# Kernel tuning notes

Measured on AMD Instinct MI355X. Metric: run time of the kernel, lower is better.

The kernel has to match this reference:

```python
import jax, jax.numpy as jnp
import numpy as np

B, F, N = 128, 256, 2000

def setup_inputs() -> dict:
    key = jax.random.key(0)
    ks = jax.random.split(key, 10)
    s = 0.05
    return {
        'nfeature': jax.random.normal(ks[0], (B, F, N, 1), jnp.float32),
        'last_current': jax.random.randint(ks[1], (B, 2), 0, N, jnp.int32),
        'Wg': jax.random.normal(ks[2], (F, F), jnp.float32) * s,
        'bg': jax.random.normal(ks[3], (F,), jnp.float32) * s,
        'Wnode': jax.random.normal(ks[4], (3 * F, F), jnp.float32) * s,
        'bnode': jax.random.normal(ks[5], (3 * F,), jnp.float32) * s,
        'Wlc': jax.random.normal(ks[6], (F, 2 * F), jnp.float32) * s,
        'blc': jax.random.normal(ks[7], (F,), jnp.float32) * s,
        'Wproj': jax.random.normal(ks[8], (F, F), jnp.float32) * s,
        'bproj': jax.random.normal(ks[9], (F,), jnp.float32) * s,
    }

def reference(nfeature, last_current, Wg, bg, Wnode, bnode, Wlc, blc, Wproj, bproj):
    # nfeature: [B, F, N, 1]
    x = nfeature[..., 0]                                  # [B, F, N]
    f = x.shape[1]
    scale = 1.0 / jnp.sqrt(jnp.asarray(f, x.dtype))
    # global fixed query: max over nodes then Linear
    glb = jnp.max(x, axis=2)                              # [B, F]
    Q = glb @ Wg.T + bg                                   # [B, F]
    # node embeddings via 1x1 conv == channel GEMM, split into K, V, logit_K
    kvl = jnp.einsum('bfn,gf->bgn', x, Wnode) + bnode[None, :, None]  # [B, 3F, N]
    K, V, Klog = jnp.split(kvl, 3, axis=1)                # each [B, F, N]
    # gather last/current city features
    lc = jnp.take_along_axis(x, last_current[:, None, :], axis=2)     # [B, F, 2]
    context = jnp.concatenate([lc[:, :, 0], lc[:, :, 1]], axis=1)     # [B, 2F]
    cQ = context @ Wlc.T + blc + Q                        # [B, F]
    # attention: single query over N keys
    ucj = jnp.einsum('bf,bfn->bn', cQ, K) * scale         # [B, N]
    attn = jax.nn.softmax(ucj, axis=1)
    nc = jnp.einsum('bn,bfn->bf', attn, V)                # [B, F]
    nc = nc @ Wproj.T + bproj                             # [B, F]
    logits = jnp.einsum('bf,bfn->bn', nc, Klog) * scale   # [B, N]
    return jnp.tanh(logits) * 10.0
```

## Files before the change

kernel.cpp:

```cpp
#include <hip/hip_runtime.h>
#include <hip/hip_fp16.h>
#include <math.h>

#define BB 128
#define FF 256
#define NN 2000

typedef float f32x4 __attribute__((ext_vector_type(4)));
union H8 { f32x4 v; __half2 h[4]; };

__global__ __launch_bounds__(256) void k_convmax(const float* __restrict__ x,
                                                 __half* __restrict__ xh,
                                                 float* __restrict__ glb) {
    int row  = (blockIdx.x << 2) | (threadIdx.x >> 6);
    int lane = threadIdx.x & 63;
    const f32x4* src = (const f32x4*)(x + (size_t)row * NN);
    f32x4*       dst = (f32x4*)(xh + (size_t)row * NN);
    float m = -INFINITY;
    for (int i = lane; i < 250; i += 64) {
        f32x4 a = __builtin_nontemporal_load(src + 2 * i);
        f32x4 b = __builtin_nontemporal_load(src + 2 * i + 1);
        m = fmaxf(m, fmaxf(fmaxf(a.x, a.y), fmaxf(a.z, a.w)));
        m = fmaxf(m, fmaxf(fmaxf(b.x, b.y), fmaxf(b.z, b.w)));
        H8 o;
        o.h[0] = __floats2half2_rn(a.x, a.y);
        o.h[1] = __floats2half2_rn(a.z, a.w);
        o.h[2] = __floats2half2_rn(b.x, b.y);
        o.h[3] = __floats2half2_rn(b.z, b.w);
        dst[i] = o.v;
    }
#pragma unroll
    for (int off = 32; off; off >>= 1) m = fmaxf(m, __shfl_xor(m, off));
    if (!lane) glb[row] = m;
}

__global__ __launch_bounds__(256) void k_prep(
    const float* __restrict__ x, const int* __restrict__ lc,
    const float* __restrict__ glb,
    const float* __restrict__ Wg, const float* __restrict__ bg,
    const float* __restrict__ Wnode, const float* __restrict__ bnode,
    const float* __restrict__ Wlc, const float* __restrict__ blc,
    float* __restrict__ cK, float* __restrict__ cK0)
{
    int b = blockIdx.x;
    int f = threadIdx.x;
    __shared__ float s_glb[FF], s_ctx[2 * FF], s_cQ[FF], s_red[FF];
    const float* xb = x + (size_t)b * FF * NN;
    s_glb[f] = glb[b * FF + f];
    int l0 = lc[2 * b], l1 = lc[2 * b + 1];
    s_ctx[f]      = xb[(size_t)f * NN + l0];
    s_ctx[FF + f] = xb[(size_t)f * NN + l1];
    __syncthreads();
    float q = bg[f];
    const float* wg = Wg + (size_t)f * FF;
    for (int j = 0; j < FF; ++j) q = fmaf(wg[j], s_glb[j], q);
    float cq = blc[f] + q;
    const float* wl = Wlc + (size_t)f * 2 * FF;
    for (int j = 0; j < 2 * FF; ++j) cq = fmaf(wl[j], s_ctx[j], cq);
    s_cQ[f]  = cq;
    s_red[f] = cq * bnode[f];
    __syncthreads();
    float ck = 0.f;
    for (int g = 0; g < FF; ++g) ck = fmaf(s_cQ[g], Wnode[(size_t)g * FF + f], ck);
    cK[b * FF + f] = ck;
    for (int s = 128; s > 0; s >>= 1) {
        if (f < s) s_red[f] += s_red[f + s];
        __syncthreads();
    }
    if (f == 0) cK0[b] = s_red[0];
}

__global__ __launch_bounds__(256) void k_ucj(const __half* __restrict__ xh,
                                             const float* __restrict__ cK,
                                             float* __restrict__ u)
{
    int b = blockIdx.x >> 2, s = blockIdx.x & 3;
    int tid = threadIdx.x, w = tid >> 6, lane = tid & 63;
    __shared__ float s_cK[FF];
    __shared__ float s_part[4][512];
    s_cK[tid] = cK[b * FF + tid];
    __syncthreads();
    int n0 = s << 9;
    int nbase = n0 + (lane << 3);
    float a0 = 0, a1 = 0, a2 = 0, a3 = 0, a4 = 0, a5 = 0, a6 = 0, a7 = 0;
    if (nbase < NN) {
        const __half* rp = xh + (size_t)(b * FF + (w << 6)) * NN + nbase;
#pragma unroll 4
        for (int fi = 0; fi < 64; ++fi) {
            H8 hv; hv.v = *(const f32x4*)rp;
            rp += NN;
            float c = s_cK[(w << 6) + fi];
            float2 q0 = __half22float2(hv.h[0]);
            float2 q1 = __half22float2(hv.h[1]);
            float2 q2 = __half22float2(hv.h[2]);
            float2 q3 = __half22float2(hv.h[3]);
            a0 = fmaf(c, q0.x, a0); a1 = fmaf(c, q0.y, a1);
            a2 = fmaf(c, q1.x, a2); a3 = fmaf(c, q1.y, a3);
            a4 = fmaf(c, q2.x, a4); a5 = fmaf(c, q2.y, a5);
            a6 = fmaf(c, q3.x, a6); a7 = fmaf(c, q3.y, a7);
        }
    }
    int cb = lane << 3;
    s_part[w][cb + 0] = a0; s_part[w][cb + 1] = a1;
    s_part[w][cb + 2] = a2; s_part[w][cb + 3] = a3;
    s_part[w][cb + 4] = a4; s_part[w][cb + 5] = a5;
    s_part[w][cb + 6] = a6; s_part[w][cb + 7] = a7;
    __syncthreads();
    for (int c = tid; c < 512; c += 256) {
        int n = n0 + c;
        if (n < NN)
            u[(size_t)b * NN + n] =
                s_part[0][c] + s_part[1][c] + s_part[2][c] + s_part[3][c];
    }
}

__global__ __launch_bounds__(256) void k_softmax(const float* __restrict__ u,
                                                 const float* __restrict__ cK0,
                                                 float* __restrict__ p)
{
    int b = blockIdx.x, tid = threadIdx.x, w = tid >> 6, lane = tid & 63;
    __shared__ float s_red[8];
    float k0 = cK0[b];
    const float scale = 0.0625f;
    float v[8];
    float m = -INFINITY;
#pragma unroll
    for (int j = 0; j < 8; ++j) {
        int n = (j << 8) + tid;
        float t = -INFINITY;
        if (n < NN) t = (u[(size_t)b * NN + n] + k0) * scale;
        v[j] = t;
        m = fmaxf(m, t);
    }
#pragma unroll
    for (int off = 32; off; off >>= 1) m = fmaxf(m, __shfl_xor(m, off));
    if (!lane) s_red[w] = m;
    __syncthreads();
    m = fmaxf(fmaxf(s_red[0], s_red[1]), fmaxf(s_red[2], s_red[3]));
    float sum = 0.f;
#pragma unroll
    for (int j = 0; j < 8; ++j) {
        float e = (v[j] > -INFINITY) ? __expf(v[j] - m) : 0.f;
        v[j] = e;
        sum += e;
    }
#pragma unroll
    for (int off = 32; off; off >>= 1) sum += __shfl_xor(sum, off);
    __syncthreads();
    if (!lane) s_red[w] = sum;
    __syncthreads();
    float inv = 1.0f / (s_red[0] + s_red[1] + s_red[2] + s_red[3]);
#pragma unroll
    for (int j = 0; j < 8; ++j) {
        int n = (j << 8) + tid;
        if (n < NN) p[(size_t)b * NN + n] = v[j] * inv;
    }
}

__global__ __launch_bounds__(256) void k_ypool(const __half* __restrict__ xh,
                                               const float* __restrict__ p,
                                               float* __restrict__ y)
{
    int b = blockIdx.x >> 4, fblk = (blockIdx.x & 15) << 4;
    int tid = threadIdx.x, w = tid >> 6, lane = tid & 63;
    const float4* pb = (const float4*)(p + (size_t)b * NN);
#pragma unroll
    for (int r = 0; r < 4; ++r) {
        int f = fblk + (w << 2) + r;
        const f32x4* row = (const f32x4*)(xh + ((size_t)b * FF + f) * NN);
        float acc = 0.f;
        for (int i = lane; i < 250; i += 64) {
            H8 hv; hv.v = row[i];
            float4 pa = pb[2 * i];
            float4 pc = pb[2 * i + 1];
            float2 q0 = __half22float2(hv.h[0]);
            float2 q1 = __half22float2(hv.h[1]);
            float2 q2 = __half22float2(hv.h[2]);
            float2 q3 = __half22float2(hv.h[3]);
            acc = fmaf(q0.x, pa.x, acc); acc = fmaf(q0.y, pa.y, acc);
            acc = fmaf(q1.x, pa.z, acc); acc = fmaf(q1.y, pa.w, acc);
            acc = fmaf(q2.x, pc.x, acc); acc = fmaf(q2.y, pc.y, acc);
            acc = fmaf(q3.x, pc.z, acc); acc = fmaf(q3.y, pc.w, acc);
        }
#pragma unroll
        for (int off = 32; off; off >>= 1) acc += __shfl_xor(acc, off);
        if (!lane) y[b * FF + f] = acc;
    }
}

__global__ __launch_bounds__(256) void k_dense(
    const float* __restrict__ y,
    const float* __restrict__ Wnode, const float* __restrict__ bnode,
    const float* __restrict__ Wproj, const float* __restrict__ bproj,
    float* __restrict__ cL, float* __restrict__ cL0)
{
    int b = blockIdx.x;
    int f = threadIdx.x;
    int wid = f >> 6, lane = f & 63;
    __shared__ float s_y[FF], s_v[FF], s_red[4];
    s_y[f] = y[b * FF + f];
    __syncthreads();
    float a = bnode[FF + f];
    const float* w = Wnode + (size_t)(FF + f) * FF;
    for (int j = 0; j < FF; ++j) a = fmaf(w[j], s_y[j], a);
    s_v[f] = a;
    __syncthreads();
    float nc2 = bproj[f];
    const float* wp = Wproj + (size_t)f * FF;
    for (int j = 0; j < FF; ++j) nc2 = fmaf(wp[j], s_v[j], nc2);
    __syncthreads();
    s_v[f] = nc2;
    __syncthreads();
    float cl = 0.f;
    for (int g = 0; g < FF; ++g) cl = fmaf(s_v[g], Wnode[(size_t)(2 * FF + g) * FF + f], cl);
    cL[b * FF + f] = cl;
    float t = nc2 * bnode[2 * FF + f];
#pragma unroll
    for (int off = 32; off; off >>= 1) t += __shfl_xor(t, off);
    if (!lane) s_red[wid] = t;
    __syncthreads();
    if (!f) cL0[b] = s_red[0] + s_red[1] + s_red[2] + s_red[3];
}

__global__ __launch_bounds__(256) void k_logits(const __half* __restrict__ xh,
                                                const float* __restrict__ cL,
                                                const float* __restrict__ cL0,
                                                float* __restrict__ out)
{
    int b = blockIdx.x >> 2, s = blockIdx.x & 3;
    int tid = threadIdx.x, w = tid >> 6, lane = tid & 63;
    __shared__ float s_cL[FF];
    __shared__ float s_part[4][512];
    s_cL[tid] = cL[b * FF + tid];
    __syncthreads();
    int n0 = s << 9;
    int nbase = n0 + (lane << 3);
    float a0 = 0, a1 = 0, a2 = 0, a3 = 0, a4 = 0, a5 = 0, a6 = 0, a7 = 0;
    if (nbase < NN) {
        const __half* rp = xh + (size_t)(b * FF + (w << 6)) * NN + nbase;
#pragma unroll 4
        for (int fi = 0; fi < 64; ++fi) {
            H8 hv; hv.v = *(const f32x4*)rp;
            rp += NN;
            float c = s_cL[(w << 6) + fi];
            float2 q0 = __half22float2(hv.h[0]);
            float2 q1 = __half22float2(hv.h[1]);
            float2 q2 = __half22float2(hv.h[2]);
            float2 q3 = __half22float2(hv.h[3]);
            a0 = fmaf(c, q0.x, a0); a1 = fmaf(c, q0.y, a1);
            a2 = fmaf(c, q1.x, a2); a3 = fmaf(c, q1.y, a3);
            a4 = fmaf(c, q2.x, a4); a5 = fmaf(c, q2.y, a5);
            a6 = fmaf(c, q3.x, a6); a7 = fmaf(c, q3.y, a7);
        }
    }
    int cb = lane << 3;
    s_part[w][cb + 0] = a0; s_part[w][cb + 1] = a1;
    s_part[w][cb + 2] = a2; s_part[w][cb + 3] = a3;
    s_part[w][cb + 4] = a4; s_part[w][cb + 5] = a5;
    s_part[w][cb + 6] = a6; s_part[w][cb + 7] = a7;
    __syncthreads();
    float cl0 = cL0[b];
    const float scale = 0.0625f;
    for (int c = tid; c < 512; c += 256) {
        int n = n0 + c;
        if (n < NN) {
            float l = (s_part[0][c] + s_part[1][c] + s_part[2][c] + s_part[3][c] + cl0) * scale;
            out[(size_t)b * NN + n] = tanhf(l) * 10.f;
        }
    }
}

extern "C" void kernel_launch(void* const* d_in, const int* in_sizes, int n_in,
                              void* d_out, int out_size, void* d_ws, size_t ws_size,
                              hipStream_t stream) {
    const float* x     = (const float*)d_in[0];
    const int*   lc    = (const int*)d_in[1];
    const float* Wg    = (const float*)d_in[2];
    const float* bg    = (const float*)d_in[3];
    const float* Wnode = (const float*)d_in[4];
    const float* bnode = (const float*)d_in[5];
    const float* Wlc   = (const float*)d_in[6];
    const float* blc   = (const float*)d_in[7];
    const float* Wproj = (const float*)d_in[8];
    const float* bproj = (const float*)d_in[9];
    float* out = (float*)d_out;

    float* ws   = (float*)d_ws;
    float* glb  = ws + 0;
    float* cK   = ws + 40960;
    float* cK0  = ws + 81920;
    float* u    = ws + 90112;
    float* p    = ws + 360448;
    float* y    = ws + 630784;
    float* cL   = ws + 663552;
    float* cL0  = ws + 696320;
    __half* xh  = (__half*)(ws + (1 << 20));

    k_convmax<<<BB * FF / 4, 256, 0, stream>>>(x, xh, glb);
    k_prep   <<<BB, 256, 0, stream>>>(x, lc, glb, Wg, bg, Wnode, bnode, Wlc, blc, cK, cK0);
    k_ucj    <<<BB * 4, 256, 0, stream>>>(xh, cK, u);
    k_softmax<<<BB, 256, 0, stream>>>(u, cK0, p);
    k_ypool  <<<BB * 16, 256, 0, stream>>>(xh, p, y);
    k_dense  <<<BB, 256, 0, stream>>>(y, Wnode, bnode, Wproj, bproj, cL, cL0);
    k_logits <<<BB * 4, 256, 0, stream>>>(xh, cL, cL0, out);
}
```

Measured before the change: 202.4 us.

## Fuse score, split softmax and pooling into one pass; fuse dense into logits

Merges the score, softmax and attention-pooling kernels into one kernel. Each block computes a local max, sum and partial pooled vector for its 512-node chunk, flash-decoding style. The final kernel combines the four partials, recomputes the dense projection chain per block and then computes the logits, which drops two launches and the u and p round trips. It also splits the accumulators in the prep matvecs. In exchange, the dense GEMVs are now recomputed four times per batch row, and the pooling loop does a 64-lane shuffle reduction for every feature row.

Measured after the change: 219.0 us. 8.2% more time.

```diff
diff --git a/kernel.cpp b/kernel.cpp
--- a/kernel.cpp
+++ b/kernel.cpp
@@ -51,18 +51,31 @@
     s_ctx[f]      = xb[(size_t)f * NN + l0];
     s_ctx[FF + f] = xb[(size_t)f * NN + l1];
     __syncthreads();
-    float q = bg[f];
     const float* wg = Wg + (size_t)f * FF;
-    for (int j = 0; j < FF; ++j) q = fmaf(wg[j], s_glb[j], q);
-    float cq = blc[f] + q;
+    float q0 = 0, q1 = 0, q2 = 0, q3 = 0;
+    for (int j = 0; j < FF; j += 4) {
+        q0 = fmaf(wg[j],     s_glb[j],     q0);
+        q1 = fmaf(wg[j + 1], s_glb[j + 1], q1);
+        q2 = fmaf(wg[j + 2], s_glb[j + 2], q2);
+        q3 = fmaf(wg[j + 3], s_glb[j + 3], q3);
+    }
     const float* wl = Wlc + (size_t)f * 2 * FF;
-    for (int j = 0; j < 2 * FF; ++j) cq = fmaf(wl[j], s_ctx[j], cq);
+    for (int j = 0; j < 2 * FF; j += 4) {
+        q0 = fmaf(wl[j],     s_ctx[j],     q0);
+        q1 = fmaf(wl[j + 1], s_ctx[j + 1], q1);
+        q2 = fmaf(wl[j + 2], s_ctx[j + 2], q2);
+        q3 = fmaf(wl[j + 3], s_ctx[j + 3], q3);
+    }
+    float cq = bg[f] + blc[f] + ((q0 + q1) + (q2 + q3));
     s_cQ[f]  = cq;
     s_red[f] = cq * bnode[f];
     __syncthreads();
-    float ck = 0.f;
-    for (int g = 0; g < FF; ++g) ck = fmaf(s_cQ[g], Wnode[(size_t)g * FF + f], ck);
-    cK[b * FF + f] = ck;
+    float c0 = 0, c1 = 0;
+    for (int g = 0; g < FF; g += 2) {
+        c0 = fmaf(s_cQ[g],     Wnode[(size_t)g * FF + f],       c0);
+        c1 = fmaf(s_cQ[g + 1], Wnode[(size_t)(g + 1) * FF + f], c1);
+    }
+    cK[b * FF + f] = c0 + c1;
     for (int s = 128; s > 0; s >>= 1) {
         if (f < s) s_red[f] += s_red[f + s];
         __syncthreads();
@@ -70,20 +83,27 @@
     if (f == 0) cK0[b] = s_red[0];
 }
 
-__global__ __launch_bounds__(256) void k_ucj(const __half* __restrict__ xh,
-                                             const float* __restrict__ cK,
-                                             float* __restrict__ u)
+__global__ __launch_bounds__(256) void k_attn(
+    const __half* __restrict__ xh,
+    const float* __restrict__ cK, const float* __restrict__ cK0,
+    float* __restrict__ y_part, float* __restrict__ m_part,
+    float* __restrict__ s_part)
 {
     int b = blockIdx.x >> 2, s = blockIdx.x & 3;
     int tid = threadIdx.x, w = tid >> 6, lane = tid & 63;
     __shared__ float s_cK[FF];
-    __shared__ float s_part[4][512];
+    __shared__ float s_acc[4][512];
+    __shared__ float s_p[512];
+    __shared__ float s_red[8];
     s_cK[tid] = cK[b * FF + tid];
     __syncthreads();
+
     int n0 = s << 9;
     int nbase = n0 + (lane << 3);
+    bool valid = nbase < NN;
+
     float a0 = 0, a1 = 0, a2 = 0, a3 = 0, a4 = 0, a5 = 0, a6 = 0, a7 = 0;
-    if (nbase < NN) {
+    if (valid) {
         const __half* rp = xh + (size_t)(b * FF + (w << 6)) * NN + nbase;
 #pragma unroll 4
         for (int fi = 0; fi < 64; ++fi) {
@@ -101,142 +121,139 @@
         }
     }
     int cb = lane << 3;
-    s_part[w][cb + 0] = a0; s_part[w][cb + 1] = a1;
-    s_part[w][cb + 2] = a2; s_part[w][cb + 3] = a3;
-    s_part[w][cb + 4] = a4; s_part[w][cb + 5] = a5;
-    s_part[w][cb + 6] = a6; s_part[w][cb + 7] = a7;
-    __syncthreads();
-    for (int c = tid; c < 512; c += 256) {
-        int n = n0 + c;
-        if (n < NN)
-            u[(size_t)b * NN + n] =
-                s_part[0][c] + s_part[1][c] + s_part[2][c] + s_part[3][c];
-    }
-}
-
-__global__ __launch_bounds__(256) void k_softmax(const float* __restrict__ u,
-                                                 const float* __restrict__ cK0,
-                                                 float* __restrict__ p)
-{
-    int b = blockIdx.x, tid = threadIdx.x, w = tid >> 6, lane = tid & 63;
-    __shared__ float s_red[8];
+    s_acc[w][cb + 0] = a0; s_acc[w][cb + 1] = a1;
+    s_acc[w][cb + 2] = a2; s_acc[w][cb + 3] = a3;
+    s_acc[w][cb + 4] = a4; s_acc[w][cb + 5] = a5;
+    s_acc[w][cb + 6] = a6; s_acc[w][cb + 7] = a7;
+    __syncthreads();
+
+    const float scale = 0.0625f;
     float k0 = cK0[b];
-    const float scale = 0.0625f;
-    float v[8];
-    float m = -INFINITY;
-#pragma unroll
-    for (int j = 0; j < 8; ++j) {
-        int n = (j << 8) + tid;
-        float t = -INFINITY;
-        if (n < NN) t = (u[(size_t)b * NN + n] + k0) * scale;
-        v[j] = t;
-        m = fmaxf(m, t);
-    }
+    float uu0, uu1;
+    {
+        int c0 = tid, c1 = tid + 256;
+        float t0 = s_acc[0][c0] + s_acc[1][c0] + s_acc[2][c0] + s_acc[3][c0];
+        float t1 = s_acc[0][c1] + s_acc[1][c1] + s_acc[2][c1] + s_acc[3][c1];
+        uu0 = (n0 + c0 < NN) ? (t0 + k0) * scale : -INFINITY;
+        uu1 = (n0 + c1 < NN) ? (t1 + k0) * scale : -INFINITY;
+    }
+    float m = fmaxf(uu0, uu1);
 #pragma unroll
     for (int off = 32; off; off >>= 1) m = fmaxf(m, __shfl_xor(m, off));
     if (!lane) s_red[w] = m;
     __syncthreads();
-    m = fmaxf(fmaxf(s_red[0], s_red[1]), fmaxf(s_red[2], s_red[3]));
-    float sum = 0.f;
-#pragma unroll
-    for (int j = 0; j < 8; ++j) {
-        float e = (v[j] > -INFINITY) ? __expf(v[j] - m) : 0.f;
-        v[j] = e;
-        sum += e;
-    }
-#pragma unroll
-    for (int off = 32; off; off >>= 1) sum += __shfl_xor(sum, off);
-    __syncthreads();
-    if (!lane) s_red[w] = sum;
-    __syncthreads();
-    float inv = 1.0f / (s_red[0] + s_red[1] + s_red[2] + s_red[3]);
-#pragma unroll
-    for (int j = 0; j < 8; ++j) {
-        int n = (j << 8) + tid;
-        if (n < NN) p[(size_t)b * NN + n] = v[j] * inv;
-    }
-}
-
-__global__ __launch_bounds__(256) void k_ypool(const __half* __restrict__ xh,
-                                               const float* __restrict__ p,
-                                               float* __restrict__ y)
-{
-    int b = blockIdx.x >> 4, fblk = (blockIdx.x & 15) << 4;
-    int tid = threadIdx.x, w = tid >> 6, lane = tid & 63;
-    const float4* pb = (const float4*)(p + (size_t)b * NN);
-#pragma unroll
-    for (int r = 0; r < 4; ++r) {
-        int f = fblk + (w << 2) + r;
-        const f32x4* row = (const f32x4*)(xh + ((size_t)b * FF + f) * NN);
+    float M = fmaxf(fmaxf(s_red[0], s_red[1]), fmaxf(s_red[2], s_red[3]));
+    float e0 = (uu0 > -INFINITY) ? __expf(uu0 - M) : 0.f;
+    float e1 = (uu1 > -INFINITY) ? __expf(uu1 - M) : 0.f;
+    s_p[tid]       = e0;
+    s_p[tid + 256] = e1;
+    float ss = e0 + e1;
+#pragma unroll
+    for (int off = 32; off; off >>= 1) ss += __shfl_xor(ss, off);
+    if (!lane) s_red[4 + w] = ss;
+    __syncthreads();
+    if (!tid) {
+        m_part[(b << 2) + s] = M;
+        s_part[(b << 2) + s] = s_red[4] + s_red[5] + s_red[6] + s_red[7];
+    }
+
+    float p0 = 0, p1 = 0, p2 = 0, p3 = 0, p4 = 0, p5 = 0, p6 = 0, p7 = 0;
+    if (valid) {
+        float4 pa = *(const float4*)&s_p[cb];
+        float4 pc = *(const float4*)&s_p[cb + 4];
+        p0 = pa.x; p1 = pa.y; p2 = pa.z; p3 = pa.w;
+        p4 = pc.x; p5 = pc.y; p6 = pc.z; p7 = pc.w;
+    }
+    const __half* rp2 = xh + (size_t)(b * FF + (w << 6)) * NN + nbase;
+    float* yp = y_part + (size_t)((b << 2) + s) * FF + (w << 6);
+#pragma unroll 2
+    for (int fi = 0; fi < 64; ++fi) {
         float acc = 0.f;
-        for (int i = lane; i < 250; i += 64) {
-            H8 hv; hv.v = row[i];
-            float4 pa = pb[2 * i];
-            float4 pc = pb[2 * i + 1];
+        if (valid) {
+            H8 hv; hv.v = *(const f32x4*)rp2;
             float2 q0 = __half22float2(hv.h[0]);
             float2 q1 = __half22float2(hv.h[1]);
             float2 q2 = __half22float2(hv.h[2]);
             float2 q3 = __half22float2(hv.h[3]);
-            acc = fmaf(q0.x, pa.x, acc); acc = fmaf(q0.y, pa.y, acc);
-            acc = fmaf(q1.x, pa.z, acc); acc = fmaf(q1.y, pa.w, acc);
-            acc = fmaf(q2.x, pc.x, acc); acc = fmaf(q2.y, pc.y, acc);
-            acc = fmaf(q3.x, pc.z, acc); acc = fmaf(q3.y, pc.w, acc);
+            acc = fmaf(p0, q0.x, acc); acc = fmaf(p1, q0.y, acc);
+            acc = fmaf(p2, q1.x, acc); acc = fmaf(p3, q1.y, acc);
+            acc = fmaf(p4, q2.x, acc); acc = fmaf(p5, q2.y, acc);
+            acc = fmaf(p6, q3.x, acc); acc = fmaf(p7, q3.y, acc);
         }
+        rp2 += NN;
 #pragma unroll
         for (int off = 32; off; off >>= 1) acc += __shfl_xor(acc, off);
-        if (!lane) y[b * FF + f] = acc;
-    }
-}
-
-__global__ __launch_bounds__(256) void k_dense(
-    const float* __restrict__ y,
+        if (!lane) yp[fi] = acc;
+    }
+}
+
+__global__ __launch_bounds__(256) void k_final(
+    const __half* __restrict__ xh,
+    const float* __restrict__ y_part, const float* __restrict__ m_part,
+    const float* __restrict__ s_part,
     const float* __restrict__ Wnode, const float* __restrict__ bnode,
     const float* __restrict__ Wproj, const float* __restrict__ bproj,
-    float* __restrict__ cL, float* __restrict__ cL0)
-{
-    int b = blockIdx.x;
-    int f = threadIdx.x;
-    int wid = f >> 6, lane = f & 63;
-    __shared__ float s_y[FF], s_v[FF], s_red[4];
-    s_y[f] = y[b * FF + f];
-    __syncthreads();
-    float a = bnode[FF + f];
-    const float* w = Wnode + (size_t)(FF + f) * FF;
-    for (int j = 0; j < FF; ++j) a = fmaf(w[j], s_y[j], a);
-    s_v[f] = a;
-    __syncthreads();
-    float nc2 = bproj[f];
-    const float* wp = Wproj + (size_t)f * FF;
-    for (int j = 0; j < FF; ++j) nc2 = fmaf(wp[j], s_v[j], nc2);
-    __syncthreads();
-    s_v[f] = nc2;
-    __syncthreads();
-    float cl = 0.f;
-    for (int g = 0; g < FF; ++g) cl = fmaf(s_v[g], Wnode[(size_t)(2 * FF + g) * FF + f], cl);
-    cL[b * FF + f] = cl;
-    float t = nc2 * bnode[2 * FF + f];
-#pragma unroll
-    for (int off = 32; off; off >>= 1) t += __shfl_xor(t, off);
-    if (!lane) s_red[wid] = t;
-    __syncthreads();
-    if (!f) cL0[b] = s_red[0] + s_red[1] + s_red[2] + s_red[3];
-}
-
-__global__ __launch_bounds__(256) void k_logits(const __half* __restrict__ xh,
-                                                const float* __restrict__ cL,
-                                                const float* __restrict__ cL0,
-                                                float* __restrict__ out)
+    float* __restrict__ out)
 {
     int b = blockIdx.x >> 2, s = blockIdx.x & 3;
     int tid = threadIdx.x, w = tid >> 6, lane = tid & 63;
-    __shared__ float s_cL[FF];
-    __shared__ float s_part[4][512];
-    s_cL[tid] = cL[b * FF + tid];
-    __syncthreads();
+    __shared__ float s_y[FF], s_v[FF], s_cL[FF];
+    __shared__ float s_acc[4][512];
+    __shared__ float s_red[8];
+
+    float m0 = m_part[(b << 2)],     m1 = m_part[(b << 2) + 1];
+    float m2 = m_part[(b << 2) + 2], m3 = m_part[(b << 2) + 3];
+    float M = fmaxf(fmaxf(m0, m1), fmaxf(m2, m3));
+    float w0 = __expf(m0 - M), w1 = __expf(m1 - M);
+    float w2 = __expf(m2 - M), w3 = __expf(m3 - M);
+    float S = s_part[(b << 2)] * w0 + s_part[(b << 2) + 1] * w1 +
+              s_part[(b << 2) + 2] * w2 + s_part[(b << 2) + 3] * w3;
+    float invS = 1.0f / S;
+    const float* yp = y_part + ((size_t)b << 2) * FF;
+    s_y[tid] = (yp[tid] * w0 + yp[FF + tid] * w1 +
+                yp[2 * FF + tid] * w2 + yp[3 * FF + tid] * w3) * invS;
+    __syncthreads();
+
+    const float* wv = Wnode + (size_t)(FF + tid) * FF;
+    float a0 = 0, a1 = 0, a2 = 0, a3 = 0;
+    for (int j = 0; j < FF; j += 4) {
+        a0 = fmaf(wv[j],     s_y[j],     a0);
+        a1 = fmaf(wv[j + 1], s_y[j + 1], a1);
+        a2 = fmaf(wv[j + 2], s_y[j + 2], a2);
+        a3 = fmaf(wv[j + 3], s_y[j + 3], a3);
+    }
+    s_v[tid] = bnode[FF + tid] + ((a0 + a1) + (a2 + a3));
+    __syncthreads();
+    const float* wp = Wproj + (size_t)tid * FF;
+    a0 = 0; a1 = 0; a2 = 0; a3 = 0;
+    for (int j = 0; j < FF; j += 4) {
+        a0 = fmaf(wp[j],     s_v[j],     a0);
+        a1 = fmaf(wp[j + 1], s_v[j + 1], a1);
+        a2 = fmaf(wp[j + 2], s_v[j + 2], a2);
+        a3 = fmaf(wp[j + 3], s_v[j + 3], a3);
+    }
+    float nc2 = bproj[tid] + ((a0 + a1) + (a2 + a3));
+    __syncthreads();
+    s_v[tid] = nc2;
+    __syncthreads();
+    float c0 = 0, c1 = 0;
+    for (int g = 0; g < FF; g += 2) {
+        c0 = fmaf(s_v[g],     Wnode[(size_t)(2 * FF + g) * FF + tid],     c0);
+        c1 = fmaf(s_v[g + 1], Wnode[(size_t)(2 * FF + g + 1) * FF + tid], c1);
+    }
+    s_cL[tid] = c0 + c1;
+    float t = nc2 * bnode[2 * FF + tid];
+#pragma unroll
+    for (int off = 32; off; off >>= 1) t += __shfl_xor(t, off);
+    if (!lane) s_red[w] = t;
+    __syncthreads();
+    float cl0 = s_red[0] + s_red[1] + s_red[2] + s_red[3];
+
     int n0 = s << 9;
     int nbase = n0 + (lane << 3);
-    float a0 = 0, a1 = 0, a2 = 0, a3 = 0, a4 = 0, a5 = 0, a6 = 0, a7 = 0;
-    if (nbase < NN) {
+    bool valid = nbase < NN;
+    float b0 = 0, b1 = 0, b2 = 0, b3 = 0, b4 = 0, b5 = 0, b6 = 0, b7 = 0;
+    if (valid) {
         const __half* rp = xh + (size_t)(b * FF + (w << 6)) * NN + nbase;
 #pragma unroll 4
         for (int fi = 0; fi < 64; ++fi) {
@@ -247,24 +264,25 @@
             float2 q1 = __half22float2(hv.h[1]);
             float2 q2 = __half22float2(hv.h[2]);
             float2 q3 = __half22float2(hv.h[3]);
-            a0 = fmaf(c, q0.x, a0); a1 = fmaf(c, q0.y, a1);
-            a2 = fmaf(c, q1.x, a2); a3 = fmaf(c, q1.y, a3);
-            a4 = fmaf(c, q2.x, a4); a5 = fmaf(c, q2.y, a5);
-            a6 = fmaf(c, q3.x, a6); a7 = fmaf(c, q3.y, a7);
+            b0 = fmaf(c, q0.x, b0); b1 = fmaf(c, q0.y, b1);
+            b2 = fmaf(c, q1.x, b2); b3 = fmaf(c, q1.y, b3);
+            b4 = fmaf(c, q2.x, b4); b5 = fmaf(c, q2.y, b5);
+            b6 = fmaf(c, q3.x, b6); b7 = fmaf(c, q3.y, b7);
         }
     }
     int cb = lane << 3;
-    s_part[w][cb + 0] = a0; s_part[w][cb + 1] = a1;
-    s_part[w][cb + 2] = a2; s_part[w][cb + 3] = a3;
-    s_part[w][cb + 4] = a4; s_part[w][cb + 5] = a5;
-    s_part[w][cb + 6] = a6; s_part[w][cb + 7] = a7;
-    __syncthreads();
-    float cl0 = cL0[b];
+    s_acc[w][cb + 0] = b0; s_acc[w][cb + 1] = b1;
+    s_acc[w][cb + 2] = b2; s_acc[w][cb + 3] = b3;
+    s_acc[w][cb + 4] = b4; s_acc[w][cb + 5] = b5;
+    s_acc[w][cb + 6] = b6; s_acc[w][cb + 7] = b7;
+    __syncthreads();
     const float scale = 0.0625f;
-    for (int c = tid; c < 512; c += 256) {
+#pragma unroll
+    for (int j = 0; j < 2; ++j) {
+        int c = tid + (j << 8);
         int n = n0 + c;
         if (n < NN) {
-            float l = (s_part[0][c] + s_part[1][c] + s_part[2][c] + s_part[3][c] + cl0) * scale;
+            float l = (s_acc[0][c] + s_acc[1][c] + s_acc[2][c] + s_acc[3][c] + cl0) * scale;
             out[(size_t)b * NN + n] = tanhf(l) * 10.f;
         }
     }
@@ -285,22 +303,17 @@
     const float* bproj = (const float*)d_in[9];
     float* out = (float*)d_out;
 
-    float* ws   = (float*)d_ws;
-    float* glb  = ws + 0;
-    float* cK   = ws + 40960;
-    float* cK0  = ws + 81920;
-    float* u    = ws + 90112;
-    float* p    = ws + 360448;
-    float* y    = ws + 630784;
-    float* cL   = ws + 663552;
-    float* cL0  = ws + 696320;
-    __half* xh  = (__half*)(ws + (1 << 20));
+    float* ws     = (float*)d_ws;
+    float* glb    = ws + 0;
+    float* cK     = ws + 40960;
+    float* cK0    = ws + 81920;
+    float* m_part = ws + 82432;
+    float* s_part = ws + 83456;
+    float* y_part = ws + 84480;
+    __half* xh    = (__half*)(ws + (1 << 20));
 
     k_convmax<<<BB * FF / 4, 256, 0, stream>>>(x, xh, glb);
     k_prep   <<<BB, 256, 0, stream>>>(x, lc, glb, Wg, bg, Wnode, bnode, Wlc, blc, cK, cK0);
-    k_ucj    <<<BB * 4, 256, 0, stream>>>(xh, cK, u);
-    k_softmax<<<BB, 256, 0, stream>>>(u, cK0, p);
-    k_ypool  <<<BB * 16, 256, 0, stream>>>(xh, p, y);
-    k_dense  <<<BB, 256, 0, stream>>>(y, Wnode, bnode, Wproj, bproj, cL, cL0);
-    k_logits <<<BB * 4, 256, 0, stream>>>(xh, cL, cL0, out);
-}
+    k_attn   <<<BB * 4, 256, 0, stream>>>(xh, cK, cK0, y_part, m_part, s_part);
+    k_final  <<<BB * 4, 256, 0, stream>>>(xh, y_part, m_part, s_part, Wnode, bnode, Wproj, bproj, out);
+}
```
